# Kernel tuning notes

Hardware: AMD Instinct MI355X
Metric: run time of the kernel (lower is better)

The kernel has to match this reference:

```python
import jax, jax.numpy as jnp
import numpy as np

B, D_IN, D_H, D_OUT = 65536, 512, 512, 512
E, N_GATE, G_H = 8, 128, 128


def _glorot(key, shape):
    bound = np.sqrt(6.0 / np.prod(shape[-2:]))
    return jax.random.uniform(key, shape, jnp.float32, -bound, bound)


def setup_inputs() -> dict:
    key = jax.random.key(0)
    ks = jax.random.split(key, 10)
    inp = {
        "z": jax.random.normal(ks[0], (B, D_IN), jnp.float32),
        "idx": jnp.arange(N_GATE, dtype=jnp.int64),
        # gating MLP (nn.Linear stored as [in, out])
        "Wg1": _glorot(ks[1], (N_GATE, G_H)), "bg1": jnp.zeros((G_H,), jnp.float32),
        "Wg2": _glorot(ks[2], (G_H, G_H)), "bg2": jnp.zeros((G_H,), jnp.float32),
        "Wg3": _glorot(ks[3], (G_H, E)), "bg3": jnp.zeros((E,), jnp.float32),
        # expert layers: W [E, in, out], b [E, out]
        "W1": _glorot(ks[4], (E, D_IN, D_H)), "b1": jnp.zeros((E, D_H), jnp.float32),
        "W2": _glorot(ks[5], (E, D_H, D_H)), "b2": jnp.zeros((E, D_H), jnp.float32),
        "W3": _glorot(ks[6], (E, D_H, D_OUT)), "b3": jnp.zeros((E, D_OUT), jnp.float32),
    }
    return inp


def _expert_layer(x, w, W, b):
    # y = sum_e w[:,e] * (x @ W[e] + b[e])  -- soft dense MoE combine
    return jnp.einsum('be,bi,eio->bo', w, x, W) + w @ b


def reference(z, idx, Wg1, bg1, Wg2, bg2, Wg3, bg3, W1, b1, W2, b2, W3, b3):
    # gating MLP on selected features (eval mode: dropout is identity)
    g = jax.nn.elu(z[:, idx] @ Wg1 + bg1)
    g = jax.nn.elu(g @ Wg2 + bg2)
    w = g @ Wg3 + bg3  # raw logits, no softmax (faithful to source)
    # experts encoder
    h = jax.nn.elu(_expert_layer(z, w, W1, b1))
    h = jax.nn.elu(_expert_layer(h, w, W2, b2))
    return _expert_layer(h, w, W3, b3)
```

## Files before the change

### kernel.cpp

```cpp
#include <hip/hip_runtime.h>

#define B_ROWS 65536

typedef __attribute__((ext_vector_type(8))) __bf16 bf16x8;
typedef __attribute__((ext_vector_type(8))) _Float16 f16x8;
typedef __attribute__((ext_vector_type(4))) float f32x4;
typedef __attribute__((ext_vector_type(8))) unsigned short u16x8;

__device__ __forceinline__ unsigned short f2bf(float f) {
  unsigned int u = __float_as_uint(f);
  u += 0x7fffu + ((u >> 16) & 1u);
  return (unsigned short)(u >> 16);
}

__device__ __forceinline__ float elu_f(float v) {
  return v > 0.f ? v : __expf(v) - 1.f;
}

__device__ __forceinline__ void async_ld16(const void* g, void* l) {
  __builtin_amdgcn_global_load_lds(
      (const __attribute__((address_space(1))) void*)g,
      (__attribute__((address_space(3))) void*)l, 16, 0, 0);
}

#define GP 136

__global__ __launch_bounds__(256) void gating_mfma(
    const float* __restrict__ z, const int* __restrict__ idx,
    const float* __restrict__ Wg1, const float* __restrict__ bg1,
    const float* __restrict__ Wg2, const float* __restrict__ bg2,
    const float* __restrict__ Wg3, const float* __restrict__ bg3,
    float* __restrict__ wq, unsigned short* __restrict__ zb) {
  __shared__ _Float16 Ab[128 * GP];
  __shared__ _Float16 Wb[128 * GP];
  __shared__ int idx_l[128];

  const int tid = threadIdx.x;
  const int lane = tid & 63, wave = tid >> 6;
  const int wr = wave >> 1, wc = wave & 1;
  const int lhi = lane >> 4, llo = lane & 15;
  const size_t row0 = (size_t)blockIdx.x * 128;

  if (tid < 128) idx_l[tid] = idx[tid];
  for (int i = tid; i < 16384; i += 256) {
    const int k = i >> 7, n = i & 127;
    Wb[n * GP + k] = (_Float16)Wg1[i];
  }
  {
    const float* zr = z + row0 * 512;
    unsigned short* zo = zb + row0 * 512;
    for (int i = tid; i < 8192; i += 256) {
      const size_t off = (size_t)i * 8;
      float4 a = *(const float4*)(zr + off);
      float4 b = *(const float4*)(zr + off + 4);
      u16x8 r;
      r[0] = f2bf(a.x); r[1] = f2bf(a.y); r[2] = f2bf(a.z); r[3] = f2bf(a.w);
      r[4] = f2bf(b.x); r[5] = f2bf(b.y); r[6] = f2bf(b.z); r[7] = f2bf(b.w);
      *(u16x8*)(zo + off) = r;
    }
  }
  __syncthreads();
  for (int i = tid; i < 16384; i += 256) {
    const int r = i >> 7, c = i & 127;
    Ab[r * GP + c] = (_Float16)z[(row0 + r) * 512 + idx_l[c]];
  }
  __syncthreads();

  const f32x4 vzero = {0.f, 0.f, 0.f, 0.f};

  f32x4 C[4][4];
#pragma unroll
  for (int i = 0; i < 4; i++)
#pragma unroll
    for (int j = 0; j < 4; j++) C[i][j] = vzero;
#pragma unroll
  for (int ks = 0; ks < 4; ks++) {
    f16x8 av[4], bv[4];
#pragma unroll
    for (int fm = 0; fm < 4; fm++)
      av[fm] = *(const f16x8*)&Ab[(wr * 64 + fm * 16 + llo) * GP + ks * 32 + lhi * 8];
#pragma unroll
    for (int fn = 0; fn < 4; fn++)
      bv[fn] = *(const f16x8*)&Wb[(wc * 64 + fn * 16 + llo) * GP + ks * 32 + lhi * 8];
#pragma unroll
    for (int fm = 0; fm < 4; fm++)
#pragma unroll
      for (int fn = 0; fn < 4; fn++)
        C[fm][fn] = __builtin_amdgcn_mfma_f32_16x16x32_f16(av[fm], bv[fn], C[fm][fn], 0, 0, 0);
  }
  __syncthreads();
#pragma unroll
  for (int fm = 0; fm < 4; fm++)
#pragma unroll
    for (int fn = 0; fn < 4; fn++) {
      const int col = wc * 64 + fn * 16 + llo;
      const float bb = bg1[col];
#pragma unroll
      for (int r = 0; r < 4; r++) {
        const int row = wr * 64 + fm * 16 + lhi * 4 + r;
        Ab[row * GP + col] = (_Float16)elu_f(C[fm][fn][r] + bb);
      }
    }
  for (int i = tid; i < 16384; i += 256) {
    const int k = i >> 7, n = i & 127;
    Wb[n * GP + k] = (_Float16)Wg2[i];
  }
  __syncthreads();

#pragma unroll
  for (int i = 0; i < 4; i++)
#pragma unroll
    for (int j = 0; j < 4; j++) C[i][j] = vzero;
#pragma unroll
  for (int ks = 0; ks < 4; ks++) {
    f16x8 av[4], bv[4];
#pragma unroll
    for (int fm = 0; fm < 4; fm++)
      av[fm] = *(const f16x8*)&Ab[(wr * 64 + fm * 16 + llo) * GP + ks * 32 + lhi * 8];
#pragma unroll
    for (int fn = 0; fn < 4; fn++)
      bv[fn] = *(const f16x8*)&Wb[(wc * 64 + fn * 16 + llo) * GP + ks * 32 + lhi * 8];
#pragma unroll
    for (int fm = 0; fm < 4; fm++)
#pragma unroll
      for (int fn = 0; fn < 4; fn++)
        C[fm][fn] = __builtin_amdgcn_mfma_f32_16x16x32_f16(av[fm], bv[fn], C[fm][fn], 0, 0, 0);
  }
  __syncthreads();
#pragma unroll
  for (int fm = 0; fm < 4; fm++)
#pragma unroll
    for (int fn = 0; fn < 4; fn++) {
      const int col = wc * 64 + fn * 16 + llo;
      const float bb = bg2[col];
#pragma unroll
      for (int r = 0; r < 4; r++) {
        const int row = wr * 64 + fm * 16 + lhi * 4 + r;
        Ab[row * GP + col] = (_Float16)elu_f(C[fm][fn][r] + bb);
      }
    }
  for (int i = tid; i < 2048; i += 256) {
    const int k = i >> 4, n = i & 15;
    Wb[n * GP + k] = (n < 8) ? (_Float16)Wg3[k * 8 + n] : (_Float16)0.f;
  }
  __syncthreads();

  f32x4 C3[4];
#pragma unroll
  for (int i = 0; i < 4; i++) C3[i] = vzero;
#pragma unroll
  for (int ks = 0; ks < 4; ks++) {
    f16x8 av[4];
#pragma unroll
    for (int fm = 0; fm < 4; fm++)
      av[fm] = *(const f16x8*)&Ab[(wr * 64 + fm * 16 + llo) * GP + ks * 32 + lhi * 8];
    const f16x8 bv = *(const f16x8*)&Wb[llo * GP + ks * 32 + lhi * 8];
#pragma unroll
    for (int fm = 0; fm < 4; fm++)
      C3[fm] = __builtin_amdgcn_mfma_f32_16x16x32_f16(av[fm], bv, C3[fm], 0, 0, 0);
  }
  if (wc == 0 && llo < 8) {
    const float bb = bg3[llo];
#pragma unroll
    for (int fm = 0; fm < 4; fm++)
#pragma unroll
      for (int r = 0; r < 4; r++) {
        const size_t row = row0 + wr * 64 + fm * 16 + lhi * 4 + r;
        wq[row * 8 + llo] = C3[fm][r] + bb;
      }
  }
}

__global__ __launch_bounds__(256) void transpose_w(
    const float* __restrict__ W1, const float* __restrict__ W2,
    const float* __restrict__ W3, unsigned short* __restrict__ Wt) {
  __shared__ float t[32][33];
  const int le = blockIdx.z;
  const float* W = (le < 8) ? W1 : (le < 16) ? W2 : W3;
  const size_t eoff = (size_t)(le & 7) * 262144;
  unsigned short* O = Wt + (size_t)le * 262144;
  const int i0 = blockIdx.y * 32, o0 = blockIdx.x * 32;
  const int tx = threadIdx.x & 31, ty = threadIdx.x >> 5;
#pragma unroll
  for (int s = 0; s < 4; s++)
    t[ty + s * 8][tx] = W[eoff + (size_t)(i0 + ty + s * 8) * 512 + o0 + tx];
  __syncthreads();
#pragma unroll
  for (int s = 0; s < 4; s++)
    O[(size_t)(o0 + ty + s * 8) * 512 + i0 + tx] = f2bf(t[tx][ty + s * 8]);
}

template <bool ELU, bool OUTBF>
__global__ __launch_bounds__(256, 2) void expert_layer(
    const unsigned short* __restrict__ X,
    const unsigned short* __restrict__ Wt,
    const float* __restrict__ bias,
    const float* __restrict__ wq,
    void* __restrict__ Out) {
  __shared__ short a_tile[128 * 64];
  __shared__ short b_tile[128 * 64];
  __shared__ float w_lds[8 * 128];
  __shared__ float bias_lds[8 * 128];

  const int tid = threadIdx.x;
  const int lane = tid & 63;
  const int wave = tid >> 6;
  const int wr = wave >> 1, wc = wave & 1;
  const int lhi = lane >> 4, llo = lane & 15;

  const int g = blockIdx.x;
  const int xcd = g & 7;
  const int s = g >> 3;
  const int nb = s & 3;
  const int mb = xcd * 64 + (s >> 2);
  const size_t row0 = (size_t)mb * 128;
  const int col0 = nb * 128;

  for (int i = tid; i < 1024; i += 256) {
    const int e = i >> 7, r = i & 127;
    w_lds[i] = wq[(row0 + r) * 8 + e];
    bias_lds[i] = bias[e * 512 + col0 + r];
  }

  const int srow = tid >> 3;
  const int cgo = ((tid & 7) ^ (srow & 7)) << 4;
  const char* Ab = (const char*)X + (row0 + srow) * 1024 + cgo;
  const char* Bb = (const char*)Wt + (size_t)(col0 + srow) * 1024 + cgo;
  char* aL = (char*)a_tile + tid * 16;
  char* bL = (char*)b_tile + tid * 16;

  const f32x4 vzero = {0.f, 0.f, 0.f, 0.f};
  f32x4 C[4][4];
#pragma unroll
  for (int i = 0; i < 4; i++)
#pragma unroll
    for (int j = 0; j < 4; j++) C[i][j] = vzero;

  const int rsw = llo & 7;

  for (int e = 0; e < 8; e++) {
    f32x4 acc[4][4];
#pragma unroll
    for (int i = 0; i < 4; i++)
#pragma unroll
      for (int j = 0; j < 4; j++) acc[i][j] = vzero;
    const char* Be = Bb + (size_t)e * 524288;
    for (int kt = 0; kt < 8; kt++) {
      const char* ga = Ab + kt * 128;
      const char* gb = Be + kt * 128;
#pragma unroll
      for (int j = 0; j < 4; j++) {
        async_ld16(ga + j * 32768, aL + j * 4096);
        async_ld16(gb + j * 32768, bL + j * 4096);
      }
      __syncthreads();
#pragma unroll
      for (int ks = 0; ks < 2; ks++) {
        const int slot = (ks * 4 + lhi) ^ rsw;
        bf16x8 av[4], bv[4];
#pragma unroll
        for (int fm = 0; fm < 4; fm++)
          av[fm] = *(const bf16x8*)((const char*)a_tile +
                                    (wr * 64 + fm * 16 + llo) * 128 + slot * 16);
#pragma unroll
        for (int fn = 0; fn < 4; fn++)
          bv[fn] = *(const bf16x8*)((const char*)b_tile +
                                    (wc * 64 + fn * 16 + llo) * 128 + slot * 16);
#pragma unroll
        for (int fm = 0; fm < 4; fm++)
#pragma unroll
          for (int fn = 0; fn < 4; fn++)
            acc[fm][fn] = __builtin_amdgcn_mfma_f32_16x16x32_bf16(
                av[fm], bv[fn], acc[fm][fn], 0, 0, 0);
      }
      __syncthreads();
    }
#pragma unroll
    for (int fm = 0; fm < 4; fm++) {
      const f32x4 wv =
          *(const f32x4*)(w_lds + e * 128 + wr * 64 + fm * 16 + lhi * 4);
#pragma unroll
      for (int fn = 0; fn < 4; fn++)
#pragma unroll
        for (int r = 0; r < 4; r++) C[fm][fn][r] += wv[r] * acc[fm][fn][r];
    }
  }

#pragma unroll
  for (int e = 0; e < 8; e++) {
    f32x4 wv[4];
#pragma unroll
    for (int fm = 0; fm < 4; fm++)
      wv[fm] = *(const f32x4*)(w_lds + e * 128 + wr * 64 + fm * 16 + lhi * 4);
#pragma unroll
    for (int fn = 0; fn < 4; fn++) {
      const float bb = bias_lds[e * 128 + wc * 64 + fn * 16 + llo];
#pragma unroll
      for (int fm = 0; fm < 4; fm++)
#pragma unroll
        for (int r = 0; r < 4; r++) C[fm][fn][r] += wv[fm][r] * bb;
    }
  }

#pragma unroll
  for (int fm = 0; fm < 4; fm++)
#pragma unroll
    for (int fn = 0; fn < 4; fn++)
#pragma unroll
      for (int r = 0; r < 4; r++) {
        float v = C[fm][fn][r];
        if (ELU) v = elu_f(v);
        const size_t orow = row0 + wr * 64 + fm * 16 + lhi * 4 + r;
        const int ocol = col0 + wc * 64 + fn * 16 + llo;
        if (OUTBF)
          ((unsigned short*)Out)[orow * 512 + ocol] = f2bf(v);
        else
          ((float*)Out)[orow * 512 + ocol] = v;
      }
}

extern "C" void kernel_launch(void* const* d_in, const int* in_sizes, int n_in,
                              void* d_out, int out_size, void* d_ws,
                              size_t ws_size, hipStream_t stream) {
  (void)in_sizes; (void)n_in; (void)out_size; (void)ws_size;
  const float* z   = (const float*)d_in[0];
  const int*   idx = (const int*)d_in[1];
  const float* Wg1 = (const float*)d_in[2];
  const float* bg1 = (const float*)d_in[3];
  const float* Wg2 = (const float*)d_in[4];
  const float* bg2 = (const float*)d_in[5];
  const float* Wg3 = (const float*)d_in[6];
  const float* bg3 = (const float*)d_in[7];
  const float* W1  = (const float*)d_in[8];
  const float* b1  = (const float*)d_in[9];
  const float* W2  = (const float*)d_in[10];
  const float* b2  = (const float*)d_in[11];
  const float* W3  = (const float*)d_in[12];
  const float* b3  = (const float*)d_in[13];

  char* ws = (char*)d_ws;
  float* wq = (float*)ws;
  unsigned short* zb = (unsigned short*)(ws + (size_t)(2u << 20));
  unsigned short* h1 = (unsigned short*)(ws + (size_t)(66u << 20));
  unsigned short* Wt = (unsigned short*)(ws + (size_t)(130u << 20));
  unsigned short* h2 = zb;

  gating_mfma<<<dim3(512), dim3(256), 0, stream>>>(
      z, idx, Wg1, bg1, Wg2, bg2, Wg3, bg3, wq, zb);
  transpose_w<<<dim3(16, 16, 24), dim3(256), 0, stream>>>(W1, W2, W3, Wt);

  expert_layer<true, true><<<dim3(2048), dim3(256), 0, stream>>>(
      zb, Wt, b1, wq, (void*)h1);
  expert_layer<true, true><<<dim3(2048), dim3(256), 0, stream>>>(
      h1, Wt + (size_t)8 * 262144, b2, wq, (void*)h2);
  expert_layer<false, false><<<dim3(2048), dim3(256), 0, stream>>>(
      h2, Wt + (size_t)16 * 262144, b3, wq, d_out);
}
```

Measured before the change: 1.141 ms.

## Pipeline expert GEMM with triple-buffered LDS and 256-row tiles over 512 threads

Rewrites the expert-layer kernel to use 512-thread blocks that cover 256x128 output tiles, so each weight tile loaded into LDS is reused across twice as many rows. The K loop becomes a triple-buffered async global-to-LDS pipeline with prefetch two steps ahead. Synchronisation is split into fine-grained s_barrier and explicit waitcnt calls, and s_setprio raises priority around the MFMA bursts. The aim is to hide global-load latency behind MFMA work and cut weight traffic, at the cost of about 144KB of LDS per block, which limits occupancy, plus fragile hand-written waitcnt counts.

```diff
diff --git a/kernel.cpp b/kernel.cpp
--- a/kernel.cpp
+++ b/kernel.cpp
@@ -191,16 +191,15 @@
 }
 
 template <bool ELU, bool OUTBF>
-__global__ __launch_bounds__(256, 2) void expert_layer(
+__global__ __launch_bounds__(512, 2) void expert_layer(
     const unsigned short* __restrict__ X,
     const unsigned short* __restrict__ Wt,
     const float* __restrict__ bias,
     const float* __restrict__ wq,
     void* __restrict__ Out) {
-  __shared__ short a_tile[128 * 64];
-  __shared__ short b_tile[128 * 64];
-  __shared__ float w_lds[8 * 128];
-  __shared__ float bias_lds[8 * 128];
+  __shared__ __align__(16) short lds[3 * 24576];
+  __shared__ __align__(16) float w_lds[8 * 256];
+  __shared__ __align__(16) float bias_lds[8 * 128];
 
   const int tid = threadIdx.x;
   const int lane = tid & 63;
@@ -210,24 +209,54 @@
 
   const int g = blockIdx.x;
   const int xcd = g & 7;
-  const int s = g >> 3;
-  const int nb = s & 3;
-  const int mb = xcd * 64 + (s >> 2);
-  const size_t row0 = (size_t)mb * 128;
+  const int sg = g >> 3;
+  const int nb = sg >> 5;
+  const int mb = xcd * 32 + (sg & 31);
+  const size_t row0 = (size_t)mb * 256;
   const int col0 = nb * 128;
 
-  for (int i = tid; i < 1024; i += 256) {
+  for (int i = tid; i < 2048; i += 512) {
+    const int e = i >> 8, r = i & 255;
+    w_lds[i] = wq[(row0 + r) * 8 + e];
+  }
+  for (int i = tid; i < 1024; i += 512) {
     const int e = i >> 7, r = i & 127;
-    w_lds[i] = wq[(row0 + r) * 8 + e];
     bias_lds[i] = bias[e * 512 + col0 + r];
   }
+  __syncthreads();
 
   const int srow = tid >> 3;
   const int cgo = ((tid & 7) ^ (srow & 7)) << 4;
-  const char* Ab = (const char*)X + (row0 + srow) * 1024 + cgo;
-  const char* Bb = (const char*)Wt + (size_t)(col0 + srow) * 1024 + cgo;
-  char* aL = (char*)a_tile + tid * 16;
-  char* bL = (char*)b_tile + tid * 16;
+  const char* Ag = (const char*)X + (row0 + srow) * 1024 + cgo;
+  const char* Bg = (const char*)Wt + (size_t)(col0 + srow) * 1024 + cgo;
+
+  auto stage = [&](int sbuf, int e, int kt, int h) {
+    const char* ga = Ag + kt * 128;
+    const char* gb = Bg + (size_t)e * 524288 + kt * 128;
+    char* lp = (char*)lds + sbuf + tid * 16;
+    if (h == 0) {
+      async_ld16(ga,          lp);
+      async_ld16(ga + 65536,  lp + 8192);
+      async_ld16(gb,          lp + 32768);
+    } else {
+      async_ld16(ga + 131072, lp + 16384);
+      async_ld16(ga + 196608, lp + 24576);
+      async_ld16(gb + 65536,  lp + 40960);
+    }
+  };
+
+  int b0 = 0, b1 = 49152, b2 = 98304;
+
+  stage(b0, 0, 0, 0); stage(b0, 0, 0, 1);
+  stage(b1, 0, 1, 0); stage(b1, 0, 1, 1);
+  asm volatile("s_waitcnt vmcnt(6)" ::: "memory");
+  __builtin_amdgcn_s_barrier();
+
+  const int rsw = llo & 7;
+  const int slot0 = (lhi ^ rsw) << 4;
+  const int slot1 = ((4 + lhi) ^ rsw) << 4;
+  const int aRow = (wr * 64 + llo) * 128;
+  const int bRow = 32768 + (wc * 64 + llo) * 128;
 
   const f32x4 vzero = {0.f, 0.f, 0.f, 0.f};
   f32x4 C[4][4];
@@ -236,49 +265,76 @@
 #pragma unroll
     for (int j = 0; j < 4; j++) C[i][j] = vzero;
 
-  const int rsw = llo & 7;
-
+  int t = 0;
+#pragma unroll 1
   for (int e = 0; e < 8; e++) {
     f32x4 acc[4][4];
 #pragma unroll
     for (int i = 0; i < 4; i++)
 #pragma unroll
       for (int j = 0; j < 4; j++) acc[i][j] = vzero;
-    const char* Be = Bb + (size_t)e * 524288;
-    for (int kt = 0; kt < 8; kt++) {
-      const char* ga = Ab + kt * 128;
-      const char* gb = Be + kt * 128;
-#pragma unroll
-      for (int j = 0; j < 4; j++) {
-        async_ld16(ga + j * 32768, aL + j * 4096);
-        async_ld16(gb + j * 32768, bL + j * 4096);
-      }
-      __syncthreads();
-#pragma unroll
-      for (int ks = 0; ks < 2; ks++) {
-        const int slot = (ks * 4 + lhi) ^ rsw;
+
+#pragma unroll 1
+    for (int kt = 0; kt < 8; kt++, t++) {
+      const int t2 = t + 2;
+      const bool more = t2 < 64;
+      const int e2 = t2 >> 3, kt2 = t2 & 7;
+      const char* base = (const char*)lds + b0;
+
+      {
         bf16x8 av[4], bv[4];
 #pragma unroll
         for (int fm = 0; fm < 4; fm++)
-          av[fm] = *(const bf16x8*)((const char*)a_tile +
-                                    (wr * 64 + fm * 16 + llo) * 128 + slot * 16);
+          av[fm] = *(const bf16x8*)(base + aRow + fm * 2048 + slot0);
 #pragma unroll
         for (int fn = 0; fn < 4; fn++)
-          bv[fn] = *(const bf16x8*)((const char*)b_tile +
-                                    (wc * 64 + fn * 16 + llo) * 128 + slot * 16);
+          bv[fn] = *(const bf16x8*)(base + bRow + fn * 2048 + slot0);
+        if (more) stage(b2, e2, kt2, 0);
+        __builtin_amdgcn_s_barrier();
+        asm volatile("s_waitcnt lgkmcnt(0)" ::: "memory");
+        __builtin_amdgcn_s_setprio(1);
 #pragma unroll
         for (int fm = 0; fm < 4; fm++)
 #pragma unroll
           for (int fn = 0; fn < 4; fn++)
             acc[fm][fn] = __builtin_amdgcn_mfma_f32_16x16x32_bf16(
                 av[fm], bv[fn], acc[fm][fn], 0, 0, 0);
-      }
-      __syncthreads();
-    }
+        __builtin_amdgcn_s_setprio(0);
+        __builtin_amdgcn_s_barrier();
+      }
+
+      {
+        bf16x8 av[4], bv[4];
+#pragma unroll
+        for (int fm = 0; fm < 4; fm++)
+          av[fm] = *(const bf16x8*)(base + aRow + fm * 2048 + slot1);
+#pragma unroll
+        for (int fn = 0; fn < 4; fn++)
+          bv[fn] = *(const bf16x8*)(base + bRow + fn * 2048 + slot1);
+        if (more) stage(b2, e2, kt2, 1);
+        __builtin_amdgcn_s_barrier();
+        asm volatile("s_waitcnt lgkmcnt(0)" ::: "memory");
+        __builtin_amdgcn_s_setprio(1);
+#pragma unroll
+        for (int fm = 0; fm < 4; fm++)
+#pragma unroll
+          for (int fn = 0; fn < 4; fn++)
+            acc[fm][fn] = __builtin_amdgcn_mfma_f32_16x16x32_bf16(
+                av[fm], bv[fn], acc[fm][fn], 0, 0, 0);
+        __builtin_amdgcn_s_setprio(0);
+        if (t < 62)
+          asm volatile("s_waitcnt vmcnt(6)" ::: "memory");
+        else
+          asm volatile("s_waitcnt vmcnt(0)" ::: "memory");
+        __builtin_amdgcn_s_barrier();
+      }
+      const int tmp = b0; b0 = b1; b1 = b2; b2 = tmp;
+    }
+
 #pragma unroll
     for (int fm = 0; fm < 4; fm++) {
       const f32x4 wv =
-          *(const f32x4*)(w_lds + e * 128 + wr * 64 + fm * 16 + lhi * 4);
+          *(const f32x4*)(w_lds + e * 256 + wr * 64 + fm * 16 + lhi * 4);
 #pragma unroll
       for (int fn = 0; fn < 4; fn++)
 #pragma unroll
@@ -291,7 +347,7 @@
     f32x4 wv[4];
 #pragma unroll
     for (int fm = 0; fm < 4; fm++)
-      wv[fm] = *(const f32x4*)(w_lds + e * 128 + wr * 64 + fm * 16 + lhi * 4);
+      wv[fm] = *(const f32x4*)(w_lds + e * 256 + wr * 64 + fm * 16 + lhi * 4);
 #pragma unroll
     for (int fn = 0; fn < 4; fn++) {
       const float bb = bias_lds[e * 128 + wc * 64 + fn * 16 + llo];
@@ -349,10 +405,10 @@
       z, idx, Wg1, bg1, Wg2, bg2, Wg3, bg3, wq, zb);
   transpose_w<<<dim3(16, 16, 24), dim3(256), 0, stream>>>(W1, W2, W3, Wt);
 
-  expert_layer<true, true><<<dim3(2048), dim3(256), 0, stream>>>(
+  expert_layer<true, true><<<dim3(1024), dim3(512), 0, stream>>>(
       zb, Wt, b1, wq, (void*)h1);
-  expert_layer<true, true><<<dim3(2048), dim3(256), 0, stream>>>(
+  expert_layer<true, true><<<dim3(1024), dim3(512), 0, stream>>>(
       h1, Wt + (size_t)8 * 262144, b2, wq, (void*)h2);
-  expert_layer<false, false><<<dim3(2048), dim3(256), 0, stream>>>(
+  expert_layer<false, false><<<dim3(1024), dim3(512), 0, stream>>>(
       h2, Wt + (size_t)16 * 262144, b3, wq, d_out);
 }
```

New measurement: 1.316 ms. +15.4%, slower.
